# Optimization experiments

Hardware: AMD Instinct MI355X
Metric: run time of the kernel (lower is better)

## Reference

```python
import jax, jax.numpy as jnp
import numpy as np

DIMS = [1024, 2048, 2048, 51]
B, P = 16, 1024


def setup_inputs() -> dict:
    key = jax.random.key(0)
    ks = jax.random.split(key, 1 + 2 * (len(DIMS) - 1))
    inp = {
        "num_pairs": P,
        "classifier_input": jax.random.normal(ks[0], (B, P, DIMS[0]), dtype=jnp.float32),
        "num_batches": B,
    }
    # Linear params, PyTorch-style: W[out, in], b[out]
    for li in range(len(DIMS) - 1):
        fan_in = DIMS[li]
        bound = 1.0 / np.sqrt(fan_in)
        inp[f"W{li}"] = jax.random.uniform(ks[1 + 2 * li], (DIMS[li + 1], fan_in), minval=-bound, maxval=bound, dtype=jnp.float32)
        inp[f"b{li}"] = jax.random.uniform(ks[2 + 2 * li], (DIMS[li + 1],), minval=-bound, maxval=bound, dtype=jnp.float32)
    return inp


def reference(num_pairs, classifier_input, num_batches, W0, b0, W1, b1, W2, b2):
    # Batched MLP over all (num_batches * num_pairs) vectors at once.
    # Original loops per (b, i); math is identical. dropout p=0.0 -> identity.
    x = classifier_input  # [B, P, d_in]
    x = jax.nn.relu(jnp.einsum("bpd,hd->bph", x, W0) + b0)
    x = jax.nn.relu(jnp.einsum("bpd,hd->bph", x, W1) + b1)
    out = jnp.einsum("bpd,od->bpo", x, W2) + b2  # [B, P, n_classes]
    return out
```

## Files before the change

### kernel.cpp

```cpp
#include <hip/hip_runtime.h>
#include <hip/hip_bf16.h>
#include <stdint.h>

typedef __attribute__((ext_vector_type(8))) short short8;
typedef __attribute__((ext_vector_type(8))) uint16_t ushort8;
typedef __attribute__((ext_vector_type(4))) float floatx4;

#define TK 64


__device__ __forceinline__ uint16_t f2bf_bits(float f) {
    uint32_t u = __builtin_bit_cast(uint32_t, f);
    u += 0x7FFFu + ((u >> 16) & 1u);
    return (uint16_t)(u >> 16);
}

__device__ __forceinline__ void async_copy16(const void* g, void* l) {
    auto gp = (const __attribute__((address_space(1))) uint32_t*)(uintptr_t)g;
    auto lp = (__attribute__((address_space(3))) uint32_t*)(uint32_t)(uintptr_t)l;
    __builtin_amdgcn_global_load_lds(gp, lp, 16, 0, 0);
}


__global__ void cvt8(const float* __restrict__ src, uint16_t* __restrict__ dst, int n) {
    int i = (blockIdx.x * 256 + threadIdx.x) * 8;
    if (i >= n) return;
    floatx4 a = *(const floatx4*)(src + i);
    floatx4 b = *(const floatx4*)(src + i + 4);
    ushort8 o;
#pragma unroll
    for (int k = 0; k < 4; k++) {
        o[k]     = f2bf_bits(a[k]);
        o[k + 4] = f2bf_bits(b[k]);
    }
    *(ushort8*)(dst + i) = o;
}

__global__ void cvt_pad_w2(const float* __restrict__ src, uint16_t* __restrict__ dst) {
    int i = (blockIdx.x * 256 + threadIdx.x) * 8;
    int row = i >> 11;
    ushort8 o;
    if (row < 51) {
        floatx4 a = *(const floatx4*)(src + i);
        floatx4 b = *(const floatx4*)(src + i + 4);
#pragma unroll
        for (int k = 0; k < 4; k++) {
            o[k]     = f2bf_bits(a[k]);
            o[k + 4] = f2bf_bits(b[k]);
        }
    } else {
#pragma unroll
        for (int k = 0; k < 8; k++) o[k] = 0;
    }
    *(ushort8*)(dst + i) = o;
}


template <int MI, int NJ, bool RELU, bool OUTF32>
__global__ __launch_bounds__(256, 2)
void gemm_bt(const uint16_t* __restrict__ A,
             const uint16_t* __restrict__ W,
             const float* __restrict__ bias,
             void* __restrict__ out,
             int M, int N, int K, int ldc, int nstore)
{
    constexpr int TMv = MI * 32;
    constexpr int TNv = NJ * 32;
    constexpr int ACH = TMv / 32;
    constexpr int BCH = TNv / 32;

    __shared__ alignas(16) uint16_t sA[TMv * TK];
    __shared__ alignas(16) uint16_t sB[TNv * TK];

    const int tid  = threadIdx.x;
    const int wave = tid >> 6;
    const int lane = tid & 63;

    const int f   = blockIdx.x;
    const int xcd = f & 7;
    const int loc = f >> 3;
    const int per = (int)gridDim.x >> 3;
    const int nt  = N / TNv;
    const int n_t = loc % nt;
    const int m_t = xcd * (per / nt) + loc / nt;
    const int n0 = n_t * TNv;
    const int m0 = m_t * TMv;

    floatx4 acc[MI][NJ];
    const floatx4 zero = {0.f, 0.f, 0.f, 0.f};
#pragma unroll
    for (int i = 0; i < MI; i++)
#pragma unroll
        for (int j = 0; j < NJ; j++) acc[i][j] = zero;

    const int wr = (wave >> 1) * MI * 16;
    const int wc = (wave & 1) * NJ * 16;

    const int sr   = lane >> 3;
    const int scol = ((lane & 7) ^ sr) * 8;

    const uint16_t* ap[ACH];
    const uint16_t* bp[BCH];
#pragma unroll
    for (int t = 0; t < ACH; t++)
        ap[t] = A + (size_t)(m0 + (wave + 4 * t) * 8 + sr) * K + scol;
#pragma unroll
    for (int t = 0; t < BCH; t++)
        bp[t] = W + (size_t)(n0 + (wave + 4 * t) * 8 + sr) * K + scol;

    const int fm = lane & 15;
    const int fr = fm & 7;
    const int kgb = lane >> 4;

    const int niter = K / TK;
    for (int it = 0; it < niter; it++) {
#pragma unroll
        for (int t = 0; t < ACH; t++) {
            async_copy16(ap[t], sA + (wave + 4 * t) * 512);
            ap[t] += TK;
        }
#pragma unroll
        for (int t = 0; t < BCH; t++) {
            async_copy16(bp[t], sB + (wave + 4 * t) * 512);
            bp[t] += TK;
        }
        __syncthreads();

#pragma unroll
        for (int kk = 0; kk < 2; kk++) {
            const int slot = ((kgb + 4 * kk) ^ fr) * 8;
            short8 af[MI], bfr[NJ];
#pragma unroll
            for (int i = 0; i < MI; i++)
                af[i] = *(const short8*)(sA + (wr + i * 16 + fm) * TK + slot);
#pragma unroll
            for (int j = 0; j < NJ; j++)
                bfr[j] = *(const short8*)(sB + (wc + j * 16 + fm) * TK + slot);
#pragma unroll
            for (int i = 0; i < MI; i++)
#pragma unroll
                for (int j = 0; j < NJ; j++)
                    acc[i][j] = __builtin_amdgcn_mfma_f32_16x16x32_bf16(af[i], bfr[j], acc[i][j], 0, 0, 0);
        }
        __syncthreads();
    }

    const int cr = (lane >> 4) * 4;
    const int cc = lane & 15;
#pragma unroll
    for (int i = 0; i < MI; i++) {
        const int gmb = m0 + wr + i * 16 + cr;
#pragma unroll
        for (int j = 0; j < NJ; j++) {
            const int gn = n0 + wc + j * 16 + cc;
            if (gn < nstore) {
                const float bv = bias[gn];
#pragma unroll
                for (int r = 0; r < 4; r++) {
                    float v = acc[i][j][r] + bv;
                    if (RELU) v = fmaxf(v, 0.f);
                    const size_t idx = (size_t)(gmb + r) * ldc + gn;
                    if (OUTF32) ((float*)out)[idx] = v;
                    else        ((uint16_t*)out)[idx] = f2bf_bits(v);
                }
            }
        }
    }
}


extern "C" void kernel_launch(void* const* d_in, const int* in_sizes, int n_in,
                              void* d_out, int out_size, void* d_ws, size_t ws_size,
                              hipStream_t stream) {
    (void)in_sizes; (void)n_in; (void)out_size; (void)ws_size;
    const float* X  = (const float*)d_in[1];
    const float* W0 = (const float*)d_in[3];
    const float* b0 = (const float*)d_in[4];
    const float* W1 = (const float*)d_in[5];
    const float* b1 = (const float*)d_in[6];
    const float* W2 = (const float*)d_in[7];
    const float* b2 = (const float*)d_in[8];

    const int M = 16384;

    char* w = (char*)d_ws;
    uint16_t* X0  = (uint16_t*)w; w += (size_t)M * 1024 * 2;
    uint16_t* X1  = (uint16_t*)w; w += (size_t)M * 2048 * 2;
    uint16_t* X2  = (uint16_t*)w; w += (size_t)M * 2048 * 2;
    uint16_t* W0b = (uint16_t*)w; w += (size_t)2048 * 1024 * 2;
    uint16_t* W1b = (uint16_t*)w; w += (size_t)2048 * 2048 * 2;
    uint16_t* W2b = (uint16_t*)w; w += (size_t)64 * 2048 * 2;

    cvt8<<<M * 1024 / 8 / 256, 256, 0, stream>>>(X, X0, M * 1024);
    cvt8<<<2048 * 1024 / 8 / 256, 256, 0, stream>>>(W0, W0b, 2048 * 1024);
    cvt8<<<2048 * 2048 / 8 / 256, 256, 0, stream>>>(W1, W1b, 2048 * 2048);
    cvt_pad_w2<<<64 * 2048 / 8 / 256, 256, 0, stream>>>(W2, W2b);

    gemm_bt<4, 8, true, false><<<dim3((M / 128) * (2048 / 256)), 256, 0, stream>>>(
        X0, W0b, b0, X1, M, 2048, 1024, 2048, 2048);
    gemm_bt<4, 8, true, false><<<dim3((M / 128) * (2048 / 256)), 256, 0, stream>>>(
        X1, W1b, b1, X2, M, 2048, 2048, 2048, 2048);
    gemm_bt<1, 2, false, true><<<dim3(M / 32), 256, 0, stream>>>(
        X2, W2b, b2, d_out, M, 64, 2048, 51, 51);
}
```

Before: 349.1 us.

## Add 256x256 double-buffered 8-wave GEMM with interleaved quadrant phases for hidden layers

Replaces the 128x256 single-buffered GEMM for the two large hidden layers with a 256x256 tile kernel using 8 waves and 128KB of dynamic LDS split into two ping-pong buffers. Each K step is broken into quadrant phases that issue the next tile's async global->LDS loads between fragment reads and MFMA bursts, using explicit waitcnt, s_barrier, setprio and sched_barrier. The goal is to overlap memory with MFMA and raise arithmetic intensity per tile. The cost is a complex, fragile hand-scheduled pipeline and lower occupancy from the large LDS footprint.

Result: slower. 369.7 us (+5.9%).

```diff
diff --git a/kernel.cpp b/kernel.cpp
--- a/kernel.cpp
+++ b/kernel.cpp
@@ -169,6 +169,190 @@
 }
 
 
+#define PH_PRE(QM, QN, SA, SB) \
+    short8 af[4][2], bf[2][2]; \
+    { const uint16_t* sAq = (SA) + (QM) * 8192 + aoff; \
+      const uint16_t* sBq = (SB) + (QN) * 8192 + boff; \
+      _Pragma("unroll") \
+      for (int kk = 0; kk < 2; kk++) { \
+        const int sl = ((kgb + 4 * kk) ^ fr) * 8; \
+        _Pragma("unroll") \
+        for (int mi = 0; mi < 4; mi++) af[mi][kk] = *(const short8*)(sAq + mi * 1024 + sl); \
+        _Pragma("unroll") \
+        for (int nj = 0; nj < 2; nj++) bf[nj][kk] = *(const short8*)(sBq + nj * 1024 + sl); \
+      } }
+
+#define PH_POST(QM, QN) \
+    __builtin_amdgcn_sched_barrier(0); \
+    __builtin_amdgcn_s_barrier(); \
+    asm volatile("s_waitcnt lgkmcnt(0)" ::: "memory"); \
+    __builtin_amdgcn_sched_barrier(0); \
+    __builtin_amdgcn_s_setprio(1); \
+    _Pragma("unroll") \
+    for (int kk = 0; kk < 2; kk++) \
+      _Pragma("unroll") \
+      for (int mi = 0; mi < 4; mi++) \
+        _Pragma("unroll") \
+        for (int nj = 0; nj < 2; nj++) \
+          acc[QM][QN][mi][nj] = __builtin_amdgcn_mfma_f32_16x16x32_bf16( \
+              af[mi][kk], bf[nj][kk], acc[QM][QN][mi][nj], 0, 0, 0); \
+    __builtin_amdgcn_s_setprio(0); \
+    __builtin_amdgcn_sched_barrier(0); \
+    __builtin_amdgcn_s_barrier(); \
+    __builtin_amdgcn_sched_barrier(0);
+
+template <bool RELU, bool OUTF32>
+__global__ __launch_bounds__(512, 2)
+void gemm256(const uint16_t* __restrict__ A,
+             const uint16_t* __restrict__ W,
+             const float* __restrict__ bias,
+             void* __restrict__ out,
+             int K, int N, int ldc, int nstore)
+{
+    extern __shared__ uint16_t smem[];
+    uint16_t* sA0 = smem;
+    uint16_t* sA1 = smem + 16384;
+    uint16_t* sB0 = smem + 32768;
+    uint16_t* sB1 = smem + 49152;
+
+    const int tid  = threadIdx.x;
+    const int wave = tid >> 6;
+    const int lane = tid & 63;
+    const int wm2  = wave >> 2;
+    const int wn2  = wave & 3;
+
+    const int f   = blockIdx.x;
+    const int xcd = f & 7;
+    const int loc = f >> 3;
+    const int per = (int)gridDim.x >> 3;
+    const int ntn = N / 256;
+    const int n_t = loc % ntn;
+    const int m_t = xcd * (per / ntn) + loc / ntn;
+    const int m0 = m_t * 256;
+    const int n0 = n_t * 256;
+
+    floatx4 acc[2][2][4][2];
+    const floatx4 zero = {0.f, 0.f, 0.f, 0.f};
+#pragma unroll
+    for (int qm = 0; qm < 2; qm++)
+#pragma unroll
+    for (int qn = 0; qn < 2; qn++)
+#pragma unroll
+    for (int mi = 0; mi < 4; mi++)
+#pragma unroll
+    for (int nj = 0; nj < 2; nj++) acc[qm][qn][mi][nj] = zero;
+
+    const int srow = lane >> 3;
+    const int scol = ((lane & 7) ^ srow) * 8;
+    const uint16_t* pA = A + (size_t)(m0 + wave * 8 + srow) * K + scol;
+    const uint16_t* pB = W + (size_t)(n0 + wave * 8 + srow) * K + scol;
+
+    auto stA = [&](int h, int kt, uint16_t* buf) {
+        const uint16_t* p = pA + (size_t)h * 128 * K + (size_t)kt * 64;
+        async_copy16(p,                 buf + h * 8192 + wave * 512);
+        async_copy16(p + (size_t)64 * K, buf + h * 8192 + 4096 + wave * 512);
+    };
+    auto stB = [&](int h, int kt, uint16_t* buf) {
+        const uint16_t* p = pB + (size_t)h * 128 * K + (size_t)kt * 64;
+        async_copy16(p,                 buf + h * 8192 + wave * 512);
+        async_copy16(p + (size_t)64 * K, buf + h * 8192 + 4096 + wave * 512);
+    };
+
+    const int fm  = lane & 15;
+    const int fr  = fm & 7;
+    const int kgb = lane >> 4;
+    const int aoff = (wm2 * 64 + fm) * 64;
+    const int boff = (wn2 * 32 + fm) * 64;
+
+    stA(0, 0, sA0);
+    stB(0, 0, sB0);
+    stA(1, 0, sA0);
+    stB(1, 0, sB0);
+    stA(0, 1, sA1);
+    stB(1, 1, sB1);
+    asm volatile("s_waitcnt vmcnt(4)" ::: "memory");
+    __builtin_amdgcn_s_barrier();
+    __builtin_amdgcn_sched_barrier(0);
+
+    const int niter2 = K / 128;
+    for (int it = 0; it < niter2; ++it) {
+        const int T = 2 * it;
+        const bool last = (it == niter2 - 1);
+
+        { PH_PRE(0, 0, sA0, sB0);
+          stB(0, T + 1, sB1);
+          asm volatile("s_waitcnt lgkmcnt(8)");
+          PH_POST(0, 0); }
+
+        { PH_PRE(0, 1, sA0, sB0);
+          stA(1, T + 1, sA1);
+          asm volatile("s_waitcnt lgkmcnt(8)");
+          PH_POST(0, 1); }
+
+        { PH_PRE(1, 1, sA0, sB0);
+          if (!last) stA(0, T + 2, sA0);
+          asm volatile("s_waitcnt lgkmcnt(8)");
+          PH_POST(1, 1); }
+
+        { PH_PRE(1, 0, sA0, sB0);
+          if (!last) stB(1, T + 2, sB0);
+          asm volatile("s_waitcnt lgkmcnt(8)");
+          if (last) asm volatile("s_waitcnt vmcnt(0)" ::: "memory");
+          else      asm volatile("s_waitcnt vmcnt(4)" ::: "memory");
+          PH_POST(1, 0); }
+
+        { PH_PRE(0, 0, sA1, sB1);
+          if (!last) stB(0, T + 2, sB0);
+          asm volatile("s_waitcnt lgkmcnt(8)");
+          PH_POST(0, 0); }
+
+        { PH_PRE(0, 1, sA1, sB1);
+          if (!last) stA(1, T + 2, sA0);
+          asm volatile("s_waitcnt lgkmcnt(8)");
+          PH_POST(0, 1); }
+
+        { PH_PRE(1, 1, sA1, sB1);
+          if (!last) stA(0, T + 3, sA1);
+          asm volatile("s_waitcnt lgkmcnt(8)");
+          PH_POST(1, 1); }
+
+        { PH_PRE(1, 0, sA1, sB1);
+          if (!last) {
+            stB(1, T + 3, sB1);
+            asm volatile("s_waitcnt lgkmcnt(8)");
+            asm volatile("s_waitcnt vmcnt(4)" ::: "memory");
+          }
+          PH_POST(1, 0); }
+    }
+
+    const int cr = (lane >> 4) * 4;
+    const int cc = lane & 15;
+#pragma unroll
+    for (int qm = 0; qm < 2; qm++)
+#pragma unroll
+    for (int mi = 0; mi < 4; mi++) {
+        const int gm = m0 + qm * 128 + wm2 * 64 + mi * 16 + cr;
+#pragma unroll
+        for (int qn = 0; qn < 2; qn++)
+#pragma unroll
+        for (int nj = 0; nj < 2; nj++) {
+            const int gn = n0 + qn * 128 + wn2 * 32 + nj * 16 + cc;
+            if (gn < nstore) {
+                const float bv = bias[gn];
+#pragma unroll
+                for (int r = 0; r < 4; r++) {
+                    float v = acc[qm][qn][mi][nj][r] + bv;
+                    if (RELU) v = fmaxf(v, 0.f);
+                    const size_t idx = (size_t)(gm + r) * ldc + gn;
+                    if (OUTF32) ((float*)out)[idx] = v;
+                    else        ((uint16_t*)out)[idx] = f2bf_bits(v);
+                }
+            }
+        }
+    }
+}
+
+
 extern "C" void kernel_launch(void* const* d_in, const int* in_sizes, int n_in,
                               void* d_out, int out_size, void* d_ws, size_t ws_size,
                               hipStream_t stream) {
@@ -183,6 +367,13 @@
 
     const int M = 16384;
 
+    static bool attr_done = false;
+    if (!attr_done) {
+        (void)hipFuncSetAttribute((const void*)gemm256<true, false>,
+                                  hipFuncAttributeMaxDynamicSharedMemorySize, 131072);
+        attr_done = true;
+    }
+
     char* w = (char*)d_ws;
     uint16_t* X0  = (uint16_t*)w; w += (size_t)M * 1024 * 2;
     uint16_t* X1  = (uint16_t*)w; w += (size_t)M * 2048 * 2;
@@ -196,10 +387,10 @@
     cvt8<<<2048 * 2048 / 8 / 256, 256, 0, stream>>>(W1, W1b, 2048 * 2048);
     cvt_pad_w2<<<64 * 2048 / 8 / 256, 256, 0, stream>>>(W2, W2b);
 
-    gemm_bt<4, 8, true, false><<<dim3((M / 128) * (2048 / 256)), 256, 0, stream>>>(
-        X0, W0b, b0, X1, M, 2048, 1024, 2048, 2048);
-    gemm_bt<4, 8, true, false><<<dim3((M / 128) * (2048 / 256)), 256, 0, stream>>>(
-        X1, W1b, b1, X2, M, 2048, 2048, 2048, 2048);
+    gemm256<true, false><<<dim3((M / 256) * (2048 / 256)), 512, 131072, stream>>>(
+        X0, W0b, b0, X1, 1024, 2048, 2048, 2048);
+    gemm256<true, false><<<dim3((M / 256) * (2048 / 256)), 512, 131072, stream>>>(
+        X1, W1b, b1, X2, 2048, 2048, 2048, 2048);
     gemm_bt<1, 2, false, true><<<dim3(M / 32), 256, 0, stream>>>(
         X2, W2b, b2, d_out, M, 64, 2048, 51, 51);
 }
```
